# Kernel optimization log

Measured on AMD Instinct MI355X. Metric: run time of the kernel, lower is better.

## Reference

```python
import jax, jax.numpy as jnp
import numpy as np

N = 100000      # nodes
E = 1600000     # edges
R = 8           # relation types
D = 128         # in_dim = h_dim = out_dim

def setup_inputs() -> dict:
    key = jax.random.key(0)
    ks = jax.random.split(key, 10)
    feats = jax.random.normal(ks[0], (N, D), dtype=jnp.float32)
    src = jax.random.randint(ks[1], (E,), 0, N, dtype=jnp.int32)
    dst = jax.random.randint(ks[2], (E,), 0, N, dtype=jnp.int32)
    etype = jax.random.randint(ks[3], (E,), 0, R, dtype=jnp.int32)
    s = 0.05  # keep activations well-scaled
    W1 = jax.random.normal(ks[4], (R, D, D), dtype=jnp.float32) * s
    loop_w1 = jax.random.normal(ks[5], (D, D), dtype=jnp.float32) * s
    b1 = jnp.zeros((D,), dtype=jnp.float32)
    W2 = jax.random.normal(ks[6], (R, D, D), dtype=jnp.float32) * s
    loop_w2 = jax.random.normal(ks[7], (D, D), dtype=jnp.float32) * s
    b2 = jnp.zeros((D,), dtype=jnp.float32)
    return {"feats": feats, "W1": W1, "loop_w1": loop_w1, "b1": b1,
            "W2": W2, "loop_w2": loop_w2, "b2": b2,
            "src": src, "dst": dst, "etype": etype}

def _rel_conv(h, W, loop_w, b, src, dst, etype, relu):
    # Per-relation transform of all node features: [R, N, out]
    # (cheaper than gathering a per-edge [E, in, out] weight tensor)
    h_rel = jnp.einsum('ni,rio->rno', h, W)
    # Per-edge message = W_{etype(e)} @ h[src(e)] : [E, out]
    msg = h_rel[etype, src]
    # Sum-aggregate messages at destination nodes
    agg = jax.ops.segment_sum(msg, dst, num_segments=h.shape[0])
    out = agg + h @ loop_w + b  # self-loop + bias
    return jax.nn.relu(out) if relu else out

def reference(feats, W1, loop_w1, b1, W2, loop_w2, b2, src, dst, etype):
    # eval-mode forward: dropout is identity
    h = _rel_conv(feats, W1, loop_w1, b1, src, dst, etype, relu=True)
    h = _rel_conv(h, W2, loop_w2, b2, src, dst, etype, relu=False)
    return h
```

## Files before the change

kernel.cpp:

```cpp
#include <hip/hip_runtime.h>
#include <hip/hip_bf16.h>


#define D 128
#define KTOT 1152
#define KACC 1024
#define BK 32
#define BSH 9
#define BSZ 512

typedef __attribute__((ext_vector_type(8))) __bf16 bf16x8;
typedef __attribute__((ext_vector_type(8))) unsigned short us8;
typedef __attribute__((ext_vector_type(4))) unsigned short us4;
typedef __attribute__((ext_vector_type(4))) float f32x4;

__device__ __forceinline__ unsigned short f2bf(float f) {
    union { float f; unsigned u; } v; v.f = f;
    unsigned r = v.u + 0x7FFF + ((v.u >> 16) & 1);
    return (unsigned short)(r >> 16);
}
__device__ __forceinline__ float bf2f(unsigned short u) {
    return __uint_as_float((unsigned)u << 16);
}

__device__ __forceinline__ int lds_off(int row, int c) {
    return row * 32 + ((c ^ ((row >> 1) & 3)) << 3);
}


__global__ __launch_bounds__(256) void histA_kernel(const int* __restrict__ dst,
                                                    int* __restrict__ bcnt, int E, int nbuck) {
    __shared__ int c[1024];
    int t = threadIdx.x;
    for (int i = t; i < nbuck; i += 256) c[i] = 0;
    __syncthreads();
    int stride = gridDim.x * 256;
    for (int e = blockIdx.x * 256 + t; e < E; e += stride)
        atomicAdd(&c[dst[e] >> BSH], 1);
    __syncthreads();
    for (int i = t; i < nbuck; i += 256)
        if (c[i]) atomicAdd(&bcnt[i], c[i]);
}

__global__ __launch_bounds__(1024) void scanA_kernel(const int* __restrict__ bcnt,
                                                     int* __restrict__ boffs,
                                                     int* __restrict__ bhead, int nbuck) {
    int t = threadIdx.x;
    int v = (t < nbuck) ? bcnt[t] : 0;
    int lane = t & 63, w = t >> 6;
    int inc = v;
    #pragma unroll
    for (int off = 1; off < 64; off <<= 1) {
        int n = __shfl_up(inc, off, 64);
        if (lane >= off) inc += n;
    }
    __shared__ int ws[16];
    if (lane == 63) ws[w] = inc;
    __syncthreads();
    int wbase = 0;
    for (int i = 0; i < w; ++i) wbase += ws[i];
    int ex = wbase + inc - v;
    if (t < nbuck) { boffs[t] = ex; bhead[t] = ex; }
    if (t == nbuck - 1) boffs[nbuck] = ex + v;
}

__global__ __launch_bounds__(256) void scatterA_kernel(const int* __restrict__ src,
                                                       const int* __restrict__ dst,
                                                       const int* __restrict__ et,
                                                       int* __restrict__ bhead,
                                                       int* __restrict__ sortedA, int E, int nbuck) {
    const int TILE = 4096;
    __shared__ int skey[TILE];
    __shared__ unsigned short sbkt[TILE];
    __shared__ int cnt[1024];
    __shared__ int lpos[1024];
    __shared__ int gdelta[1024];
    __shared__ int ws[4];
    const int t = threadIdx.x;
    const int e0 = blockIdx.x * TILE;
    int dreg[16];

    for (int i = t; i < nbuck; i += 256) cnt[i] = 0;
    __syncthreads();
    #pragma unroll
    for (int j = 0; j < 16; ++j) {
        int e = e0 + j * 256 + t;
        int d = -1;
        if (e < E) { d = dst[e]; atomicAdd(&cnt[d >> BSH], 1); }
        dreg[j] = d;
    }
    __syncthreads();
    int b0 = t * 4;
    int c0 = 0, c1 = 0, c2 = 0, c3 = 0;
    if (b0     < nbuck) c0 = cnt[b0];
    if (b0 + 1 < nbuck) c1 = cnt[b0 + 1];
    if (b0 + 2 < nbuck) c2 = cnt[b0 + 2];
    if (b0 + 3 < nbuck) c3 = cnt[b0 + 3];
    int s = c0 + c1 + c2 + c3;
    int lane = t & 63, w = t >> 6;
    int inc = s;
    #pragma unroll
    for (int off = 1; off < 64; off <<= 1) {
        int n = __shfl_up(inc, off, 64);
        if (lane >= off) inc += n;
    }
    if (lane == 63) ws[w] = inc;
    __syncthreads();
    int wbase = 0;
    for (int i = 0; i < w; ++i) wbase += ws[i];
    int ex = wbase + inc - s;
    int l0 = ex, l1 = ex + c0, l2 = ex + c0 + c1, l3 = ex + c0 + c1 + c2;
    if (b0     < nbuck) { lpos[b0]     = l0; if (c0) gdelta[b0]     = atomicAdd(&bhead[b0],     c0) - l0; }
    if (b0 + 1 < nbuck) { lpos[b0 + 1] = l1; if (c1) gdelta[b0 + 1] = atomicAdd(&bhead[b0 + 1], c1) - l1; }
    if (b0 + 2 < nbuck) { lpos[b0 + 2] = l2; if (c2) gdelta[b0 + 2] = atomicAdd(&bhead[b0 + 2], c2) - l2; }
    if (b0 + 3 < nbuck) { lpos[b0 + 3] = l3; if (c3) gdelta[b0 + 3] = atomicAdd(&bhead[b0 + 3], c3) - l3; }
    __syncthreads();
    #pragma unroll
    for (int j = 0; j < 16; ++j) {
        int e = e0 + j * 256 + t;
        if (e < E) {
            int d = dreg[j];
            int b = d >> BSH;
            int key = ((d & (BSZ - 1)) << 20) | (et[e] << 17) | src[e];
            int p = atomicAdd(&lpos[b], 1);
            skey[p] = key;
            sbkt[p] = (unsigned short)b;
        }
    }
    __syncthreads();
    int ntile = min(TILE, E - e0);
    for (int i = t; i < ntile; i += 256)
        sortedA[gdelta[sbkt[i]] + i] = skey[i];
}


__global__ __launch_bounds__(256) void passB_kernel(const int* __restrict__ sortedA,
                                                    const int* __restrict__ boffs,
                                                    int* __restrict__ sorted,
                                                    int* __restrict__ offs2,
                                                    int N8, int E, int nbuck) {
    __shared__ int cnt[4096];
    __shared__ int cur[4096];
    __shared__ int ws[4];
    const int b = blockIdx.x;
    const int t = threadIdx.x;
    const int gb0 = boffs[b], gb1 = boffs[b + 1];
    #pragma unroll
    for (int i = 0; i < 16; ++i) cnt[i * 256 + t] = 0;
    __syncthreads();
    for (int e = gb0 + t; e < gb1; e += 256) {
        int k = sortedA[e];
        atomicAdd(&cnt[(k >> 17) & 4095], 1);
    }
    __syncthreads();
    const int base = t * 16;
    int s = 0;
    #pragma unroll
    for (int i = 0; i < 16; ++i) s += cnt[base + i];
    int lane = t & 63, w = t >> 6;
    int inc = s;
    #pragma unroll
    for (int off = 1; off < 64; off <<= 1) {
        int n = __shfl_up(inc, off, 64);
        if (lane >= off) inc += n;
    }
    if (lane == 63) ws[w] = inc;
    __syncthreads();
    int wbase = 0;
    for (int i = 0; i < w; ++i) wbase += ws[i];
    int run = gb0 + wbase + inc - s;
    int g0 = (b << 12) + base;
    #pragma unroll
    for (int i = 0; i < 16; ++i) {
        int cv = cnt[base + i];
        cur[base + i] = run;
        if (g0 + i <= N8) offs2[g0 + i] = run;
        run += cv;
    }
    __syncthreads();
    for (int e = gb0 + t; e < gb1; e += 256) {
        int k = sortedA[e];
        int p = atomicAdd(&cur[(k >> 17) & 4095], 1);
        sorted[p] = k;
    }
}


__global__ void cast_kernel(const float* __restrict__ W1, const float* __restrict__ lw1,
                            const float* __restrict__ W2, const float* __restrict__ lw2,
                            const float* __restrict__ feats,
                            unsigned short* __restrict__ Bt1, unsigned short* __restrict__ Bt2,
                            unsigned short* __restrict__ hb0, int n4) {
    const int per = KTOT * D;
    int idx = blockIdx.x * blockDim.x + threadIdx.x;
    if (idx < 2 * per) {
        int layer = idx / per;
        int rem = idx - layer * per;
        int k = rem >> 7;
        int o = rem & 127;
        const float* W  = layer ? W2 : W1;
        const float* lw = layer ? lw2 : lw1;
        float val = (k < 1024) ? W[k * D + o] : lw[(k - 1024) * D + o];
        unsigned short* Bt = layer ? Bt2 : Bt1;
        Bt[o * KTOT + k] = f2bf(val);
    } else {
        int i = idx - 2 * per;
        if (i < n4) {
            float4 v = *(const float4*)(feats + (size_t)i * 4);
            us4 o; o.x = f2bf(v.x); o.y = f2bf(v.y); o.z = f2bf(v.z); o.w = f2bf(v.w);
            *(us4*)(hb0 + (size_t)i * 4) = o;
        }
    }
}


__global__ __launch_bounds__(256) void aggregate_kernel(const unsigned short* __restrict__ hb,
                                                        const int* __restrict__ offs2,
                                                        const int* __restrict__ sorted,
                                                        unsigned short* __restrict__ A,
                                                        int v0, int vend) {
    const int t = threadIdx.x;
    const int u = t >> 4;
    const int c = (t & 15) * 8;
    const int v = v0 + blockIdx.x * 16 + u;
    if (v >= vend) return;

    const int* o2 = offs2 + (size_t)v * 8;
    unsigned short* Ab = A + (size_t)(v - v0) * KACC + c;
    int e0 = o2[0];
    #pragma unroll
    for (int r = 0; r < 8; ++r) {
        int e1 = o2[r + 1];
        float a[8];
        #pragma unroll
        for (int j = 0; j < 8; ++j) a[j] = 0.f;
        #pragma unroll 2
        for (int e = e0; e < e1; ++e) {
            int p = sorted[e];
            int s = p & 131071;
            us8 hv = *(const us8*)(hb + (size_t)s * D + c);
            #pragma unroll
            for (int j = 0; j < 8; ++j) a[j] += bf2f(hv[j]);
        }
        us8 o;
        #pragma unroll
        for (int j = 0; j < 8; ++j) o[j] = f2bf(a[j]);
        *(us8*)(Ab + r * 128) = o;
        e0 = e1;
    }
}


__global__ __launch_bounds__(256) void gemm_kernel(const unsigned short* __restrict__ A,
                                                   const unsigned short* __restrict__ hbA,
                                                   const unsigned short* __restrict__ Bt,
                                                   const float* __restrict__ bias,
                                                   float* __restrict__ outf,
                                                   unsigned short* __restrict__ outb,
                                                   int v0, int vend, int relu_bf) {
    __shared__ unsigned short Alds[128 * 32];
    __shared__ unsigned short Blds[128 * 32];
    const int t = threadIdx.x;
    const int lane = t & 63;
    const int w = t >> 6;
    const int quad = lane >> 4;
    const int c16 = lane & 15;
    const int blockRow0 = v0 + blockIdx.x * 128;

    const int srow = t >> 2;
    const int schunk = t & 3;

    f32x4 acc[2][8];
    #pragma unroll
    for (int i = 0; i < 2; ++i)
        #pragma unroll
        for (int j = 0; j < 8; ++j) acc[i][j] = f32x4{0.f, 0.f, 0.f, 0.f};

    const int aRow0 = blockRow0 + srow;
    const int aRow1 = blockRow0 + srow + 64;
    const bool val0 = aRow0 < vend;
    const bool val1 = aRow1 < vend;
    const us8 zz = {0, 0, 0, 0, 0, 0, 0, 0};

    for (int k0 = 0; k0 < KTOT; k0 += BK) {
        us8 av0 = zz, av1 = zz;
        if (k0 < KACC) {
            if (val0) av0 = *(const us8*)(A + (size_t)(aRow0 - v0) * KACC + k0 + schunk * 8);
            if (val1) av1 = *(const us8*)(A + (size_t)(aRow1 - v0) * KACC + k0 + schunk * 8);
        } else {
            if (val0) av0 = *(const us8*)(hbA + (size_t)aRow0 * D + (k0 - KACC) + schunk * 8);
            if (val1) av1 = *(const us8*)(hbA + (size_t)aRow1 * D + (k0 - KACC) + schunk * 8);
        }
        us8 bv0 = *(const us8*)(Bt + (size_t)srow * KTOT + k0 + schunk * 8);
        us8 bv1 = *(const us8*)(Bt + (size_t)(srow + 64) * KTOT + k0 + schunk * 8);
        __syncthreads();
        *(us8*)(Alds + lds_off(srow,      schunk)) = av0;
        *(us8*)(Alds + lds_off(srow + 64, schunk)) = av1;
        *(us8*)(Blds + lds_off(srow,      schunk)) = bv0;
        *(us8*)(Blds + lds_off(srow + 64, schunk)) = bv1;
        __syncthreads();

        bf16x8 af[2];
        #pragma unroll
        for (int rt = 0; rt < 2; ++rt)
            af[rt] = *(const bf16x8*)(Alds + lds_off(w * 32 + rt * 16 + c16, quad));
        #pragma unroll
        for (int ct = 0; ct < 8; ++ct) {
            bf16x8 bfr = *(const bf16x8*)(Blds + lds_off(ct * 16 + c16, quad));
            acc[0][ct] = __builtin_amdgcn_mfma_f32_16x16x32_bf16(af[0], bfr, acc[0][ct], 0, 0, 0);
            acc[1][ct] = __builtin_amdgcn_mfma_f32_16x16x32_bf16(af[1], bfr, acc[1][ct], 0, 0, 0);
        }
    }

    #pragma unroll
    for (int rt = 0; rt < 2; ++rt) {
        int row = blockRow0 + w * 32 + rt * 16 + quad * 4;
        #pragma unroll
        for (int ct = 0; ct < 8; ++ct) {
            int col = ct * 16 + c16;
            float bcol = bias[col];
            #pragma unroll
            for (int i = 0; i < 4; ++i) {
                int r = row + i;
                if (r < vend) {
                    float vv = acc[rt][ct][i] + bcol;
                    if (relu_bf) {
                        vv = fmaxf(vv, 0.f);
                        outb[(size_t)r * D + col] = f2bf(vv);
                    } else {
                        outf[(size_t)r * D + col] = vv;
                    }
                }
            }
        }
    }
}


extern "C" void kernel_launch(void* const* d_in, const int* in_sizes, int n_in,
                              void* d_out, int out_size, void* d_ws, size_t ws_size,
                              hipStream_t stream) {
    const float* feats = (const float*)d_in[0];
    const float* W1    = (const float*)d_in[1];
    const float* lw1   = (const float*)d_in[2];
    const float* b1    = (const float*)d_in[3];
    const float* W2    = (const float*)d_in[4];
    const float* lw2   = (const float*)d_in[5];
    const float* b2    = (const float*)d_in[6];
    const int*   src   = (const int*)d_in[7];
    const int*   dst   = (const int*)d_in[8];
    const int*   etype = (const int*)d_in[9];
    const int N = in_sizes[0] / D;
    const int E = in_sizes[7];
    float* out = (float*)d_out;

    const int ch = (N + 1) / 2;
    const int nbuck = (N + BSZ - 1) >> BSH;

    size_t woff = 0;
    auto take = [&](size_t bytes) -> void* {
        void* p = (char*)d_ws + woff;
        woff += (bytes + 255) & ~(size_t)255;
        return p;
    };
    int* bcnt           = (int*)take((size_t)1024 * 4);
    int* boffs          = (int*)take((size_t)1025 * 4);
    int* bhead          = (int*)take((size_t)1024 * 4);
    int* offs2          = (int*)take((size_t)(N * 8 + 1) * 4);
    int* sortedA        = (int*)take((size_t)E * 4);
    int* sorted         = (int*)take((size_t)E * 4);
    unsigned short* Bt1 = (unsigned short*)take((size_t)KTOT * D * 2);
    unsigned short* Bt2 = (unsigned short*)take((size_t)KTOT * D * 2);
    unsigned short* hb0 = (unsigned short*)take((size_t)N * D * 2);
    unsigned short* hb1 = (unsigned short*)take((size_t)N * D * 2);
    unsigned short* ACC = (unsigned short*)take((size_t)ch * KACC * 2);

    (void)hipMemsetAsync(bcnt, 0, (size_t)nbuck * 4, stream);

    histA_kernel<<<1024, 256, 0, stream>>>(dst, bcnt, E, nbuck);
    scanA_kernel<<<1, 1024, 0, stream>>>(bcnt, boffs, bhead, nbuck);
    scatterA_kernel<<<(E + 4095) / 4096, 256, 0, stream>>>(src, dst, etype, bhead, sortedA, E, nbuck);
    passB_kernel<<<nbuck, 256, 0, stream>>>(sortedA, boffs, sorted, offs2, N * 8, E, nbuck);

    int n4 = N * D / 4;
    int cb = (2 * KTOT * D + n4 + 255) / 256;
    cast_kernel<<<cb, 256, 0, stream>>>(W1, lw1, W2, lw2, feats, Bt1, Bt2, hb0, n4);

    for (int layer = 0; layer < 2; ++layer) {
        const unsigned short* hin = layer ? hb1 : hb0;
        const unsigned short* Bt  = layer ? Bt2 : Bt1;
        const float* bias         = layer ? b2  : b1;
        for (int c0 = 0; c0 < N; c0 += ch) {
            int c1 = (c0 + ch < N) ? (c0 + ch) : N;
            int len = c1 - c0;
            int ab = (len + 15) / 16;
            int gb = (len + 127) / 128;
            aggregate_kernel<<<ab, 256, 0, stream>>>(hin, offs2, sorted, ACC, c0, c1);
            gemm_kernel<<<gb, 256, 0, stream>>>(ACC, hin, Bt, bias, out, hb1, c0, c1, 1 - layer);
        }
    }
}
```

Before: 576.0 us.

## Halve GEMM row tile to 64 and prefetch next K-slice into registers

The GEMM block tile shrinks from 128 to 64 rows, so each wave computes one 16-row MFMA tile instead of two and the grid doubles. Global loads for the next K step are issued before the LDS stores and MFMAs of the current step, giving register double-buffering that hides load latency. The aim is more blocks to fill the GPU for small chunks, and overlap of memory with compute. The cost is that B-tile loads per output row double and each B fragment is reused by only one MFMA instead of two.

```diff
diff --git a/kernel.cpp b/kernel.cpp
--- a/kernel.cpp
+++ b/kernel.cpp
@@ -258,78 +258,76 @@
                                                    float* __restrict__ outf,
                                                    unsigned short* __restrict__ outb,
                                                    int v0, int vend, int relu_bf) {
-    __shared__ unsigned short Alds[128 * 32];
+    __shared__ unsigned short Alds[64 * 32];
     __shared__ unsigned short Blds[128 * 32];
     const int t = threadIdx.x;
     const int lane = t & 63;
     const int w = t >> 6;
     const int quad = lane >> 4;
     const int c16 = lane & 15;
-    const int blockRow0 = v0 + blockIdx.x * 128;
+    const int blockRow0 = v0 + blockIdx.x * 64;
 
     const int srow = t >> 2;
     const int schunk = t & 3;
 
-    f32x4 acc[2][8];
-    #pragma unroll
-    for (int i = 0; i < 2; ++i)
-        #pragma unroll
-        for (int j = 0; j < 8; ++j) acc[i][j] = f32x4{0.f, 0.f, 0.f, 0.f};
-
-    const int aRow0 = blockRow0 + srow;
-    const int aRow1 = blockRow0 + srow + 64;
-    const bool val0 = aRow0 < vend;
-    const bool val1 = aRow1 < vend;
+    f32x4 acc[8];
+    #pragma unroll
+    for (int j = 0; j < 8; ++j) acc[j] = f32x4{0.f, 0.f, 0.f, 0.f};
+
+    const int aRow = blockRow0 + srow;
+    const bool aval = aRow < vend;
     const us8 zz = {0, 0, 0, 0, 0, 0, 0, 0};
+    const unsigned short* Arow = A + (size_t)(aRow - v0) * KACC + schunk * 8;
+    const unsigned short* Hrow = hbA + (size_t)aRow * D + schunk * 8;
+    const unsigned short* Brow0 = Bt + (size_t)srow * KTOT + schunk * 8;
+    const unsigned short* Brow1 = Bt + (size_t)(srow + 64) * KTOT + schunk * 8;
+
+    us8 av = zz;
+    if (aval) av = *(const us8*)(Arow);
+    us8 bv0 = *(const us8*)(Brow0);
+    us8 bv1 = *(const us8*)(Brow1);
 
     for (int k0 = 0; k0 < KTOT; k0 += BK) {
-        us8 av0 = zz, av1 = zz;
-        if (k0 < KACC) {
-            if (val0) av0 = *(const us8*)(A + (size_t)(aRow0 - v0) * KACC + k0 + schunk * 8);
-            if (val1) av1 = *(const us8*)(A + (size_t)(aRow1 - v0) * KACC + k0 + schunk * 8);
-        } else {
-            if (val0) av0 = *(const us8*)(hbA + (size_t)aRow0 * D + (k0 - KACC) + schunk * 8);
-            if (val1) av1 = *(const us8*)(hbA + (size_t)aRow1 * D + (k0 - KACC) + schunk * 8);
-        }
-        us8 bv0 = *(const us8*)(Bt + (size_t)srow * KTOT + k0 + schunk * 8);
-        us8 bv1 = *(const us8*)(Bt + (size_t)(srow + 64) * KTOT + k0 + schunk * 8);
+        us8 na = zz, nb0 = zz, nb1 = zz;
+        const int kn = k0 + BK;
+        if (kn < KTOT) {
+            if (aval) {
+                if (kn < KACC) na = *(const us8*)(Arow + kn);
+                else           na = *(const us8*)(Hrow + (kn - KACC));
+            }
+            nb0 = *(const us8*)(Brow0 + kn);
+            nb1 = *(const us8*)(Brow1 + kn);
+        }
         __syncthreads();
-        *(us8*)(Alds + lds_off(srow,      schunk)) = av0;
-        *(us8*)(Alds + lds_off(srow + 64, schunk)) = av1;
+        *(us8*)(Alds + lds_off(srow, schunk)) = av;
         *(us8*)(Blds + lds_off(srow,      schunk)) = bv0;
         *(us8*)(Blds + lds_off(srow + 64, schunk)) = bv1;
         __syncthreads();
 
-        bf16x8 af[2];
-        #pragma unroll
-        for (int rt = 0; rt < 2; ++rt)
-            af[rt] = *(const bf16x8*)(Alds + lds_off(w * 32 + rt * 16 + c16, quad));
+        bf16x8 af = *(const bf16x8*)(Alds + lds_off(w * 16 + c16, quad));
         #pragma unroll
         for (int ct = 0; ct < 8; ++ct) {
             bf16x8 bfr = *(const bf16x8*)(Blds + lds_off(ct * 16 + c16, quad));
-            acc[0][ct] = __builtin_amdgcn_mfma_f32_16x16x32_bf16(af[0], bfr, acc[0][ct], 0, 0, 0);
-            acc[1][ct] = __builtin_amdgcn_mfma_f32_16x16x32_bf16(af[1], bfr, acc[1][ct], 0, 0, 0);
-        }
-    }
-
-    #pragma unroll
-    for (int rt = 0; rt < 2; ++rt) {
-        int row = blockRow0 + w * 32 + rt * 16 + quad * 4;
+            acc[ct] = __builtin_amdgcn_mfma_f32_16x16x32_bf16(af, bfr, acc[ct], 0, 0, 0);
+        }
+        av = na; bv0 = nb0; bv1 = nb1;
+    }
+
+    int row = blockRow0 + w * 16 + quad * 4;
+    #pragma unroll
+    for (int ct = 0; ct < 8; ++ct) {
+        int col = ct * 16 + c16;
+        float bcol = bias[col];
         #pragma unroll
-        for (int ct = 0; ct < 8; ++ct) {
-            int col = ct * 16 + c16;
-            float bcol = bias[col];
-            #pragma unroll
-            for (int i = 0; i < 4; ++i) {
-                int r = row + i;
-                if (r < vend) {
-                    float vv = acc[rt][ct][i] + bcol;
-                    if (relu_bf) {
-                        vv = fmaxf(vv, 0.f);
-                        outb[(size_t)r * D + col] = f2bf(vv);
-                    } else {
-                        outf[(size_t)r * D + col] = vv;
-                    }
+        for (int i = 0; i < 4; ++i) {
+            int r = row + i;
+            if (r < vend) {
+                float vv = acc[ct][i] + bcol;
+                if (relu_bf) {
+                    vv = fmaxf(vv, 0.f);
+                    outb[(size_t)r * D + col] = f2bf(vv);
+                } else {
+                    outf[(size_t)r * D + col] = vv;
                 }
             }
         }
@@ -394,7 +392,7 @@
             int c1 = (c0 + ch < N) ? (c0 + ch) : N;
             int len = c1 - c0;
             int ab = (len + 15) / 16;
-            int gb = (len + 127) / 128;
+            int gb = (len + 63) / 64;
             aggregate_kernel<<<ab, 256, 0, stream>>>(hin, offs2, sorted, ACC, c0, c1);
             gemm_kernel<<<gb, 256, 0, stream>>>(ACC, hin, Bt, bias, out, hb1, c0, c1, 1 - layer);
         }
```

After: 575.4 us. Within noise of the previous version (-0.1%).
